# Kernel tuning notes

Measured on AMD Instinct MI355X. Metric: run time of the kernel, lower is better.

Reference implementation:

```python
import jax, jax.numpy as jnp
import numpy as np

T, B, IN, H, L = 512, 64, 1024, 1024, 2


def setup_inputs() -> dict:
    key = jax.random.key(0)
    ks = jax.random.split(key, 9)
    stdv = 1.0 / np.sqrt(H)
    u = lambda k, shape: jax.random.uniform(k, shape, jnp.float32, -stdv, stdv)
    return {
        "x": jax.random.normal(ks[0], (T, B, IN), jnp.float32),
        "h0": jnp.zeros((L, B, H), jnp.float32),
        "w_ih_l0": u(ks[1], (3 * H, IN)),
        "w_hh_l0": u(ks[2], (3 * H, H)),
        "b_ih_l0": u(ks[3], (3 * H,)),
        "b_hh_l0": u(ks[4], (3 * H,)),
        "w_ih_l1": u(ks[5], (3 * H, H)),
        "w_hh_l1": u(ks[6], (3 * H, H)),
        "b_ih_l1": u(ks[7], (3 * H,)),
        "b_hh_l1": u(ks[8], (3 * H,)),
    }


def _gru_layer(x, h, w_ih, w_hh, b_ih, b_hh):
    # Precompute input-side gates for all timesteps: [T, B, 3H]
    gx = jnp.einsum('tbi,gi->tbg', x, w_ih) + b_ih

    def step(h_prev, gx_t):
        gh = h_prev @ w_hh.T + b_hh  # [B, 3H]
        gxr, gxz, gxn = jnp.split(gx_t, 3, axis=-1)
        ghr, ghz, ghn = jnp.split(gh, 3, axis=-1)
        r = jax.nn.sigmoid(gxr + ghr)
        z = jax.nn.sigmoid(gxz + ghz)
        n = jnp.tanh(gxn + r * ghn)
        h_new = n + z * (h_prev - n)
        return h_new, h_new

    h_last, ys = jax.lax.scan(step, h, gx)
    return ys, h_last


def reference(x, h0, w_ih_l0, w_hh_l0, b_ih_l0, b_hh_l0,
              w_ih_l1, w_hh_l1, b_ih_l1, b_hh_l1):
    y0, hn0 = _gru_layer(x, h0[0], w_ih_l0, w_hh_l0, b_ih_l0, b_hh_l0)
    y1, hn1 = _gru_layer(y0, h0[1], w_ih_l1, w_hh_l1, b_ih_l1, b_hh_l1)
    return y1, jnp.stack([hn0, hn1], axis=0)
```

## Files before the change

### kernel.cpp

```cpp
#include <hip/hip_runtime.h>
#include <hip/hip_bf16.h>
#include <math.h>

#define T_STEPS 512
#define BATCH   64
#define HID     1024
#define G3      3072
#define BH      (BATCH * HID)

typedef __attribute__((ext_vector_type(8))) short          bf16x8;
typedef __attribute__((ext_vector_type(8))) unsigned short u16x8;
typedef __attribute__((ext_vector_type(4))) float          f32x4;

__device__ inline unsigned short f2bf(float f) {
    __hip_bfloat16 h = __float2bfloat16(f);
    return *reinterpret_cast<unsigned short*>(&h);
}

__device__ inline bf16x8 load_h8(const unsigned short* p) {
    typedef unsigned long long u64;
    u64 lo = __hip_atomic_load((const u64*)p,       __ATOMIC_RELAXED, __HIP_MEMORY_SCOPE_AGENT);
    u64 hi = __hip_atomic_load((const u64*)(p + 4), __ATOMIC_RELAXED, __HIP_MEMORY_SCOPE_AGENT);
    union { u64 q[2]; bf16x8 v; } u;
    u.q[0] = lo; u.q[1] = hi;
    return u.v;
}

__device__ inline float fast_sigmoid(float x) {
    return __builtin_amdgcn_rcpf(1.f + __expf(-x));
}
__device__ inline float fast_tanh(float x) {
    float e = __expf(-2.f * fabsf(x));
    float t = (1.f - e) * __builtin_amdgcn_rcpf(1.f + e);
    return copysignf(t, x);
}

__global__ void cvt_f32_bf16(const float* __restrict__ src,
                             unsigned short* __restrict__ dst, int n)
{
    int i = (blockIdx.x * blockDim.x + threadIdx.x) * 4;
    if (i + 3 < n) {
        float4 v = *(const float4*)(src + i);
        ushort4 o;
        o.x = f2bf(v.x); o.y = f2bf(v.y); o.z = f2bf(v.z); o.w = f2bf(v.w);
        *(ushort4*)(dst + i) = o;
    }
}

__global__ __launch_bounds__(256) void gemm_gx_bf16(
    const float* __restrict__ A, const unsigned short* __restrict__ Wbf,
    const float* __restrict__ bias, float* __restrict__ C, int M)
{
    __shared__ unsigned short As[128][72];
    __shared__ unsigned short Bs[128][72];
    const int tid = threadIdx.x;
    const int l  = tid & 63;
    const int w  = tid >> 6;
    const int wm = w >> 1, wn = w & 1;
    const int m0 = blockIdx.y * 128, n0 = blockIdx.x * 128;
    const int lr = l & 15, lk = (l >> 4) * 8;

    f32x4 acc[4][4] = {};

    const int arow = tid >> 4, acol = (tid & 15) * 4;
    const int brow = tid >> 3, bcol = (tid & 7) * 8;

    for (int k0 = 0; k0 < 1024; k0 += 64) {
        float4 av[8];
        #pragma unroll
        for (int r = 0; r < 8; ++r)
            av[r] = *(const float4*)(A + (size_t)(m0 + r * 16 + arow) * 1024 + k0 + acol);
        u16x8 bv[4];
        #pragma unroll
        for (int r = 0; r < 4; ++r)
            bv[r] = *(const u16x8*)(Wbf + (size_t)(n0 + r * 32 + brow) * 1024 + k0 + bcol);

        __syncthreads();
        #pragma unroll
        for (int r = 0; r < 8; ++r) {
            ushort4 o;
            o.x = f2bf(av[r].x); o.y = f2bf(av[r].y);
            o.z = f2bf(av[r].z); o.w = f2bf(av[r].w);
            *(ushort4*)&As[r * 16 + arow][acol] = o;
        }
        #pragma unroll
        for (int r = 0; r < 4; ++r)
            *(u16x8*)&Bs[r * 32 + brow][bcol] = bv[r];
        __syncthreads();

        #pragma unroll
        for (int kk = 0; kk < 2; ++kk) {
            bf16x8 af[4], bfr[4];
            #pragma unroll
            for (int i = 0; i < 4; ++i)
                af[i] = *(const bf16x8*)&As[wm * 64 + i * 16 + lr][kk * 32 + lk];
            #pragma unroll
            for (int j = 0; j < 4; ++j)
                bfr[j] = *(const bf16x8*)&Bs[wn * 64 + j * 16 + lr][kk * 32 + lk];
            #pragma unroll
            for (int i = 0; i < 4; ++i)
                #pragma unroll
                for (int j = 0; j < 4; ++j)
                    acc[i][j] = __builtin_amdgcn_mfma_f32_16x16x32_bf16(
                        af[i], bfr[j], acc[i][j], 0, 0, 0);
        }
    }

    #pragma unroll
    for (int j = 0; j < 4; ++j) {
        const int col = n0 + wn * 64 + j * 16 + lr;
        const float bv = bias[col];
        #pragma unroll
        for (int i = 0; i < 4; ++i) {
            const int rb = m0 + wm * 64 + i * 16 + (l >> 4) * 4;
            #pragma unroll
            for (int r = 0; r < 4; ++r)
                C[(size_t)(rb + r) * G3 + col] = acc[i][j][r] + bv;
        }
    }
}

__global__ __launch_bounds__(256, 1) void gru_persist(
    const float* __restrict__ gx,
    unsigned short* __restrict__ hbf,
    const float* __restrict__ hprev0,
    const unsigned short* __restrict__ whh,
    const float* __restrict__ bhh,
    float* __restrict__ y_all,
    unsigned int* __restrict__ flags,
    int step_base, int t0, int tc)
{
    __shared__ float red[4][64][13];

    const int tid = threadIdx.x;
    const int bid = blockIdx.x;
    const int jt = bid & 63;
    const int bg = bid >> 6;
    const int l  = tid & 63;
    const int w  = tid >> 6;
    const int lr = l & 15, lk = (l >> 4) * 8;

    const unsigned short* hpb = hbf + (size_t)(bg * 16 + lr) * HID + w * 256 + lk;
    const unsigned short* wr  = whh + (size_t)(jt * 16 + lr) * HID + w * 256 + lk;
    const unsigned short* wz  = wr + (size_t)HID * HID;
    const unsigned short* wn  = wz + (size_t)HID * HID;

    bf16x8 wvr[8], wvz[8], wvn[8];
    #pragma unroll
    for (int kc = 0; kc < 8; ++kc) {
        wvr[kc] = *(const bf16x8*)(wr + kc * 32);
        wvz[kc] = *(const bf16x8*)(wz + kc * 32);
        wvn[kc] = *(const bf16x8*)(wn + kc * 32);
    }

    const int q  = tid >> 6;
    const int fl = tid & 63;
    const int j  = jt * 16 + (fl & 15);
    const int b  = bg * 16 + 4 * (fl >> 4) + q;
    const float brc = bhh[j], bzc = bhh[HID + j], bnc = bhh[2 * HID + j];
    float hreg = hprev0[(size_t)b * HID + j];

    float gxr = gx[(size_t)b * G3 + j];
    float gxz = gx[(size_t)b * G3 + HID + j];
    float gxn = gx[(size_t)b * G3 + 2 * HID + j];

    for (int ts = 0; ts < tc; ++ts) {
        const int t = t0 + ts;
        const size_t coff = (size_t)(t & 1) * BH;
        const size_t noff = (size_t)((t + 1) & 1) * BH;
        const unsigned int stamp = (unsigned int)(step_base + ts + 1);

        f32x4 ar = {0.f, 0.f, 0.f, 0.f};
        f32x4 az = {0.f, 0.f, 0.f, 0.f};
        f32x4 an = {0.f, 0.f, 0.f, 0.f};
        #pragma unroll
        for (int kc = 0; kc < 8; ++kc) {
            bf16x8 a = load_h8(hpb + coff + kc * 32);
            ar = __builtin_amdgcn_mfma_f32_16x16x32_bf16(a, wvr[kc], ar, 0, 0, 0);
            az = __builtin_amdgcn_mfma_f32_16x16x32_bf16(a, wvz[kc], az, 0, 0, 0);
            an = __builtin_amdgcn_mfma_f32_16x16x32_bf16(a, wvn[kc], an, 0, 0, 0);
        }
        #pragma unroll
        for (int i = 0; i < 4; ++i) {
            red[w][l][i]     = ar[i];
            red[w][l][4 + i] = az[i];
            red[w][l][8 + i] = an[i];
        }
        __syncthreads();

        float sr = 0.f, sz = 0.f, sn = 0.f;
        #pragma unroll
        for (int s = 0; s < 4; ++s) {
            sr += red[s][fl][q];
            sz += red[s][fl][4 + q];
            sn += red[s][fl][8 + q];
        }
        const float rg = fast_sigmoid(gxr + sr + brc);
        const float zg = fast_sigmoid(gxz + sz + bzc);
        const float ng = fast_tanh(gxn + rg * (sn + bnc));
        hreg = ng + zg * (hreg - ng);

        unsigned int myu = (unsigned int)f2bf(hreg);
        unsigned int pu  = __shfl_xor(myu, 1);
        if (!(fl & 1))
            __hip_atomic_store((unsigned int*)(hbf + noff + (size_t)b * HID + j),
                               myu | (pu << 16),
                               __ATOMIC_RELAXED, __HIP_MEMORY_SCOPE_AGENT);

        __syncthreads();
        if (tid == 0)
            __hip_atomic_store(&flags[bg * 64 + jt], stamp,
                               __ATOMIC_RELAXED, __HIP_MEMORY_SCOPE_AGENT);

        y_all[(size_t)t * BH + (size_t)b * HID + j] = hreg;
        const int tsn = (ts + 1 < tc) ? ts + 1 : ts;
        const float* gxp = gx + (size_t)tsn * BATCH * G3;
        const float ngxr = gxp[(size_t)b * G3 + j];
        const float ngxz = gxp[(size_t)b * G3 + HID + j];
        const float ngxn = gxp[(size_t)b * G3 + 2 * HID + j];

        if (tid < 64) {
            for (;;) {
                unsigned int f = __hip_atomic_load(&flags[bg * 64 + tid],
                                                   __ATOMIC_RELAXED,
                                                   __HIP_MEMORY_SCOPE_AGENT);
                if (__ballot(f >= stamp) == ~0ull) break;
                __builtin_amdgcn_s_sleep(1);
            }
        }
        __syncthreads();
        gxr = ngxr; gxz = ngxz; gxn = ngxn;
    }
}

__global__ void copy_f32(const float* __restrict__ src, float* __restrict__ dst, int n)
{
    int i = blockIdx.x * blockDim.x + threadIdx.x;
    if (i < n) dst[i] = src[i];
}

extern "C" void kernel_launch(void* const* d_in, const int* in_sizes, int n_in,
                              void* d_out, int out_size, void* d_ws, size_t ws_size,
                              hipStream_t stream)
{
    const float* x    = (const float*)d_in[0];
    const float* h0   = (const float*)d_in[1];
    const float* wih[2] = {(const float*)d_in[2], (const float*)d_in[6]};
    const float* whh[2] = {(const float*)d_in[3], (const float*)d_in[7]};
    const float* bih[2] = {(const float*)d_in[4], (const float*)d_in[8]};
    const float* bhh[2] = {(const float*)d_in[5], (const float*)d_in[9]};

    float* out = (float*)d_out;
    float* y   = out;
    float* hn  = out + (size_t)T_STEPS * BH;

    const size_t WSZ = (size_t)G3 * HID;
    unsigned short* wsu = (unsigned short*)d_ws;
    unsigned short* whh_bf[2] = {wsu, wsu + WSZ};
    unsigned short* wih_bf[2] = {wsu + 2 * WSZ, wsu + 3 * WSZ};
    unsigned short* hbf = wsu + 4 * WSZ;
    unsigned int* flags = (unsigned int*)(wsu + 4 * WSZ + 2 * (size_t)BH);
    const size_t FLAG_N = 4 * 64;
    float* gx = (float*)((char*)flags + FLAG_N * sizeof(unsigned int));
    const size_t fixed_bytes = (4 * WSZ + 2 * (size_t)BH) * 2 + FLAG_N * 4;
    const size_t gx_bytes = ws_size > fixed_bytes ? ws_size - fixed_bytes : 0;

    int TC = 512;
    while (TC > 2 && (size_t)TC * BATCH * G3 * 4 > gx_bytes) TC >>= 1;

    hipMemsetAsync(flags, 0, FLAG_N * sizeof(unsigned int), stream);

    for (int layer = 0; layer < 2; ++layer) {
        cvt_f32_bf16<<<(int)(WSZ / 1024), 256, 0, stream>>>(whh[layer], whh_bf[layer], (int)WSZ);
        cvt_f32_bf16<<<(int)(WSZ / 1024), 256, 0, stream>>>(wih[layer], wih_bf[layer], (int)WSZ);
    }

    for (int layer = 0; layer < 2; ++layer) {
        const float* A_all = (layer == 0) ? x : y;
        const float* hinit = h0 + (size_t)layer * BH;

        cvt_f32_bf16<<<BH / 1024, 256, 0, stream>>>(hinit, hbf, BH);

        for (int c0 = 0; c0 < T_STEPS; c0 += TC) {
            dim3 ggrid(G3 / 128, TC * BATCH / 128);
            gemm_gx_bf16<<<ggrid, 256, 0, stream>>>(
                A_all + (size_t)c0 * BH, wih_bf[layer], bih[layer],
                gx, TC * BATCH);

            const float* gxp = gx;
            const float* hprev0 = (c0 == 0) ? hinit : (y + (size_t)(c0 - 1) * BH);
            const unsigned short* whhp = whh_bf[layer];
            const float* bhhp = bhh[layer];
            float* yp = y;
            unsigned short* hbfp = hbf;
            unsigned int* flp = flags;
            int sb = layer * T_STEPS + c0;
            int t0v = c0, tcv = TC;
            void* kargs[] = {(void*)&gxp, (void*)&hbfp, (void*)&hprev0,
                             (void*)&whhp, (void*)&bhhp, (void*)&yp,
                             (void*)&flp, (void*)&sb, (void*)&t0v, (void*)&tcv};
            hipLaunchCooperativeKernel((const void*)gru_persist,
                                       dim3(256), dim3(256), kargs, 0, stream);
        }
        copy_f32<<<(BH + 255) / 256, 256, 0, stream>>>(
            y + (size_t)(T_STEPS - 1) * BH, hn + (size_t)layer * BH, BH);
    }
}
```

Baseline: 5.778 ms.

## Stage recurrent weights in LDS and use lighter custom barriers in GRU loop

The recurrent weight tiles for each block, previously held in registers (72 VGPRs per lane), are now staged once into shared memory and read from LDS on every timestep. The __syncthreads calls in the step loop become raw s_barrier calls with explicit waitcnt, so a barrier only waits on the counter it actually needs. This frees registers and cuts barrier overhead, at the cost of extra LDS reads on the critical recurrent path. The weaker fences also rely on the vmcnt wait before the flag store to keep the h writes ordered ahead of the flag.

After: 7.546 ms. 1.31x slower.

```diff
diff --git a/kernel.cpp b/kernel.cpp
--- a/kernel.cpp
+++ b/kernel.cpp
@@ -11,6 +11,7 @@
 typedef __attribute__((ext_vector_type(8))) short          bf16x8;
 typedef __attribute__((ext_vector_type(8))) unsigned short u16x8;
 typedef __attribute__((ext_vector_type(4))) float          f32x4;
+typedef unsigned long long u64;
 
 __device__ inline unsigned short f2bf(float f) {
     __hip_bfloat16 h = __float2bfloat16(f);
@@ -18,7 +19,6 @@
 }
 
 __device__ inline bf16x8 load_h8(const unsigned short* p) {
-    typedef unsigned long long u64;
     u64 lo = __hip_atomic_load((const u64*)p,       __ATOMIC_RELAXED, __HIP_MEMORY_SCOPE_AGENT);
     u64 hi = __hip_atomic_load((const u64*)(p + 4), __ATOMIC_RELAXED, __HIP_MEMORY_SCOPE_AGENT);
     union { u64 q[2]; bf16x8 v; } u;
@@ -33,6 +33,16 @@
     float e = __expf(-2.f * fabsf(x));
     float t = (1.f - e) * __builtin_amdgcn_rcpf(1.f + e);
     return copysignf(t, x);
+}
+
+__device__ inline void bar_lgkm() {
+    asm volatile("s_waitcnt lgkmcnt(0)" ::: "memory");
+    __builtin_amdgcn_s_barrier();
+    __builtin_amdgcn_sched_barrier(0);
+}
+__device__ inline void bar_only() {
+    __builtin_amdgcn_s_barrier();
+    __builtin_amdgcn_sched_barrier(0);
 }
 
 __global__ void cvt_f32_bf16(const float* __restrict__ src,
@@ -130,39 +140,47 @@
     unsigned int* __restrict__ flags,
     int step_base, int t0, int tc)
 {
+    __shared__ unsigned short wlds[3 * 4 * 8 * 4 * 16 * 8];
     __shared__ float red[4][64][13];
 
     const int tid = threadIdx.x;
     const int bid = blockIdx.x;
     const int jt = bid & 63;
     const int bg = bid >> 6;
-    const int l  = tid & 63;
-    const int w  = tid >> 6;
-    const int lr = l & 15, lk = (l >> 4) * 8;
-
-    const unsigned short* hpb = hbf + (size_t)(bg * 16 + lr) * HID + w * 256 + lk;
-    const unsigned short* wr  = whh + (size_t)(jt * 16 + lr) * HID + w * 256 + lk;
-    const unsigned short* wz  = wr + (size_t)HID * HID;
-    const unsigned short* wn  = wz + (size_t)HID * HID;
-
-    bf16x8 wvr[8], wvz[8], wvn[8];
+    const int l   = tid & 63;
+    const int ks  = tid >> 6;
+    const int lr  = l & 15;
+    const int lgrp = l >> 4;
+
     #pragma unroll
-    for (int kc = 0; kc < 8; ++kc) {
-        wvr[kc] = *(const bf16x8*)(wr + kc * 32);
-        wvz[kc] = *(const bf16x8*)(wz + kc * 32);
-        wvn[kc] = *(const bf16x8*)(wn + kc * 32);
-    }
+    for (int i = 0; i < 24; ++i) {
+        int vi  = tid + i * 256;
+        int slr = vi & 15;
+        int slg = (vi >> 4) & 3;
+        int skc = (vi >> 6) & 7;
+        int sks = (vi >> 9) & 3;
+        int sg  = vi >> 11;
+        u16x8 wv = *(const u16x8*)(whh
+            + ((size_t)(sg * HID + jt * 16 + slr) << 10)
+            + sks * 256 + skc * 32 + slg * 8);
+        *(u16x8*)&wlds[(size_t)vi * 8] = wv;
+    }
+
+    const unsigned short* hpb = hbf + (size_t)(bg * 16 + lr) * HID + ks * 256 + lgrp * 8;
+    const int wbase = (ks * 8) * 64 + lgrp * 16 + lr;
 
     const int q  = tid >> 6;
     const int fl = tid & 63;
     const int j  = jt * 16 + (fl & 15);
     const int b  = bg * 16 + 4 * (fl >> 4) + q;
-    const float brc = bhh[j], bzc = bhh[HID + j], bnc = bhh[2 * HID + j];
+    const float bhr = bhh[j], bhz = bhh[HID + j], bhn = bhh[2 * HID + j];
     float hreg = hprev0[(size_t)b * HID + j];
 
     float gxr = gx[(size_t)b * G3 + j];
     float gxz = gx[(size_t)b * G3 + HID + j];
     float gxn = gx[(size_t)b * G3 + 2 * HID + j];
+
+    bar_lgkm();
 
     for (int ts = 0; ts < tc; ++ts) {
         const int t = t0 + ts;
@@ -175,18 +193,21 @@
         f32x4 an = {0.f, 0.f, 0.f, 0.f};
         #pragma unroll
         for (int kc = 0; kc < 8; ++kc) {
-            bf16x8 a = load_h8(hpb + coff + kc * 32);
-            ar = __builtin_amdgcn_mfma_f32_16x16x32_bf16(a, wvr[kc], ar, 0, 0, 0);
-            az = __builtin_amdgcn_mfma_f32_16x16x32_bf16(a, wvz[kc], az, 0, 0, 0);
-            an = __builtin_amdgcn_mfma_f32_16x16x32_bf16(a, wvn[kc], an, 0, 0, 0);
+            bf16x8 a  = load_h8(hpb + coff + kc * 32);
+            bf16x8 Br = *(const bf16x8*)&wlds[(size_t)(wbase + kc * 64) * 8];
+            bf16x8 Bz = *(const bf16x8*)&wlds[(size_t)(2048 + wbase + kc * 64) * 8];
+            bf16x8 Bn = *(const bf16x8*)&wlds[(size_t)(4096 + wbase + kc * 64) * 8];
+            ar = __builtin_amdgcn_mfma_f32_16x16x32_bf16(a, Br, ar, 0, 0, 0);
+            az = __builtin_amdgcn_mfma_f32_16x16x32_bf16(a, Bz, az, 0, 0, 0);
+            an = __builtin_amdgcn_mfma_f32_16x16x32_bf16(a, Bn, an, 0, 0, 0);
         }
         #pragma unroll
         for (int i = 0; i < 4; ++i) {
-            red[w][l][i]     = ar[i];
-            red[w][l][4 + i] = az[i];
-            red[w][l][8 + i] = an[i];
-        }
-        __syncthreads();
+            red[ks][l][i]     = ar[i];
+            red[ks][l][4 + i] = az[i];
+            red[ks][l][8 + i] = an[i];
+        }
+        bar_lgkm();
 
         float sr = 0.f, sz = 0.f, sn = 0.f;
         #pragma unroll
@@ -195,9 +216,9 @@
             sz += red[s][fl][4 + q];
             sn += red[s][fl][8 + q];
         }
-        const float rg = fast_sigmoid(gxr + sr + brc);
-        const float zg = fast_sigmoid(gxz + sz + bzc);
-        const float ng = fast_tanh(gxn + rg * (sn + bnc));
+        const float rg = fast_sigmoid(gxr + sr + bhr);
+        const float zg = fast_sigmoid(gxz + sz + bhz);
+        const float ng = fast_tanh(gxn + rg * (sn + bhn));
         hreg = ng + zg * (hreg - ng);
 
         unsigned int myu = (unsigned int)f2bf(hreg);
@@ -207,7 +228,8 @@
                                myu | (pu << 16),
                                __ATOMIC_RELAXED, __HIP_MEMORY_SCOPE_AGENT);
 
-        __syncthreads();
+        asm volatile("s_waitcnt vmcnt(0)" ::: "memory");
+        bar_only();
         if (tid == 0)
             __hip_atomic_store(&flags[bg * 64 + jt], stamp,
                                __ATOMIC_RELAXED, __HIP_MEMORY_SCOPE_AGENT);
@@ -228,7 +250,7 @@
                 __builtin_amdgcn_s_sleep(1);
             }
         }
-        __syncthreads();
+        bar_only();
         gxr = ngxr; gxz = ngxz; gxn = ngxn;
     }
 }
```

## Fuse both GRU layers into one wavefront-pipelined persistent kernel

Applied to the files above, without the earlier changes.

Replaces the two per-layer persistent recurrences with a single cooperative kernel in which layer 1 runs one timestep behind layer 0. This roughly halves the number of serial grid-wide barrier steps. Layer 1's input projection is computed inline from the bf16 layer-0 hidden state with MFMA, so the second large input GEMM disappears. In exchange, recurrent weights are no longer kept in registers and are reloaded from memory every step, which adds per-step memory traffic and more MFMA work per step. Final hidden states are written directly, and chunk-boundary state is carried through workspace buffers.

New measurement: 7.957 ms. 37.7% more time.

```diff
diff --git a/kernel.cpp b/kernel.cpp
--- a/kernel.cpp
+++ b/kernel.cpp
@@ -11,6 +11,7 @@
 typedef __attribute__((ext_vector_type(8))) short          bf16x8;
 typedef __attribute__((ext_vector_type(8))) unsigned short u16x8;
 typedef __attribute__((ext_vector_type(4))) float          f32x4;
+typedef unsigned long long u64;
 
 __device__ inline unsigned short f2bf(float f) {
     __hip_bfloat16 h = __float2bfloat16(f);
@@ -18,7 +19,6 @@
 }
 
 __device__ inline bf16x8 load_h8(const unsigned short* p) {
-    typedef unsigned long long u64;
     u64 lo = __hip_atomic_load((const u64*)p,       __ATOMIC_RELAXED, __HIP_MEMORY_SCOPE_AGENT);
     u64 hi = __hip_atomic_load((const u64*)(p + 4), __ATOMIC_RELAXED, __HIP_MEMORY_SCOPE_AGENT);
     union { u64 q[2]; bf16x8 v; } u;
@@ -120,101 +120,174 @@
     }
 }
 
-__global__ __launch_bounds__(256, 1) void gru_persist(
-    const float* __restrict__ gx,
-    unsigned short* __restrict__ hbf,
-    const float* __restrict__ hprev0,
-    const unsigned short* __restrict__ whh,
-    const float* __restrict__ bhh,
-    float* __restrict__ y_all,
+__global__ __launch_bounds__(256, 1) void gru_pipe(
+    const float* __restrict__ gx0,
+    unsigned short* __restrict__ hbf0,
+    unsigned short* __restrict__ hbf1,
+    const float* __restrict__ h0f_in,
+    const float* __restrict__ h1f_in,
+    float* __restrict__ h0f_out,
+    float* __restrict__ h1f_out,
+    const unsigned short* __restrict__ whh0,
+    const unsigned short* __restrict__ wih1,
+    const unsigned short* __restrict__ whh1,
+    const float* __restrict__ bhh0,
+    const float* __restrict__ bih1,
+    const float* __restrict__ bhh1,
+    float* __restrict__ y1_all,
+    float* __restrict__ hn,
     unsigned int* __restrict__ flags,
-    int step_base, int t0, int tc)
+    int c0, int tc)
 {
-    __shared__ float red[4][64][13];
+    __shared__ float red[4][64][29];
 
     const int tid = threadIdx.x;
     const int bid = blockIdx.x;
     const int jt = bid & 63;
     const int bg = bid >> 6;
-    const int l  = tid & 63;
-    const int w  = tid >> 6;
-    const int lr = l & 15, lk = (l >> 4) * 8;
-
-    const unsigned short* hpb = hbf + (size_t)(bg * 16 + lr) * HID + w * 256 + lk;
-    const unsigned short* wr  = whh + (size_t)(jt * 16 + lr) * HID + w * 256 + lk;
-    const unsigned short* wz  = wr + (size_t)HID * HID;
-    const unsigned short* wn  = wz + (size_t)HID * HID;
-
-    bf16x8 wvr[8], wvz[8], wvn[8];
-    #pragma unroll
-    for (int kc = 0; kc < 8; ++kc) {
-        wvr[kc] = *(const bf16x8*)(wr + kc * 32);
-        wvz[kc] = *(const bf16x8*)(wz + kc * 32);
-        wvn[kc] = *(const bf16x8*)(wn + kc * 32);
-    }
+    const int l   = tid & 63;
+    const int ks  = tid >> 6;
+    const int lr  = l & 15;
+    const int lgrp = l >> 4;
+
+    const unsigned short* hpb0 = hbf0 + (size_t)(bg * 16 + lr) * HID + ks * 256 + lgrp * 8;
+    const unsigned short* hpb1 = hbf1 + (size_t)(bg * 16 + lr) * HID + ks * 256 + lgrp * 8;
+
+    const size_t basew = ((size_t)(jt * 16 + lr) << 10) + ks * 256 + lgrp * 8;
+    const size_t GS = (size_t)HID * HID;
+    const unsigned short* w0 = whh0 + basew;
+    const unsigned short* wi = wih1 + basew;
+    const unsigned short* wh = whh1 + basew;
 
     const int q  = tid >> 6;
     const int fl = tid & 63;
     const int j  = jt * 16 + (fl & 15);
     const int b  = bg * 16 + 4 * (fl >> 4) + q;
-    const float brc = bhh[j], bzc = bhh[HID + j], bnc = bhh[2 * HID + j];
-    float hreg = hprev0[(size_t)b * HID + j];
-
-    float gxr = gx[(size_t)b * G3 + j];
-    float gxz = gx[(size_t)b * G3 + HID + j];
-    float gxn = gx[(size_t)b * G3 + 2 * HID + j];
-
-    for (int ts = 0; ts < tc; ++ts) {
-        const int t = t0 + ts;
-        const size_t coff = (size_t)(t & 1) * BH;
-        const size_t noff = (size_t)((t + 1) & 1) * BH;
-        const unsigned int stamp = (unsigned int)(step_base + ts + 1);
-
-        f32x4 ar = {0.f, 0.f, 0.f, 0.f};
-        f32x4 az = {0.f, 0.f, 0.f, 0.f};
-        f32x4 an = {0.f, 0.f, 0.f, 0.f};
-        #pragma unroll
-        for (int kc = 0; kc < 8; ++kc) {
-            bf16x8 a = load_h8(hpb + coff + kc * 32);
-            ar = __builtin_amdgcn_mfma_f32_16x16x32_bf16(a, wvr[kc], ar, 0, 0, 0);
-            az = __builtin_amdgcn_mfma_f32_16x16x32_bf16(a, wvz[kc], az, 0, 0, 0);
-            an = __builtin_amdgcn_mfma_f32_16x16x32_bf16(a, wvn[kc], an, 0, 0, 0);
-        }
-        #pragma unroll
-        for (int i = 0; i < 4; ++i) {
-            red[w][l][i]     = ar[i];
-            red[w][l][4 + i] = az[i];
-            red[w][l][8 + i] = an[i];
-        }
-        __syncthreads();
-
-        float sr = 0.f, sz = 0.f, sn = 0.f;
+    const float b0r = bhh0[j], b0z = bhh0[HID + j], b0n = bhh0[2 * HID + j];
+    const float b1r = bih1[j] + bhh1[j];
+    const float b1z = bih1[HID + j] + bhh1[HID + j];
+    const float b1ni = bih1[2 * HID + j];
+    const float b1nh = bhh1[2 * HID + j];
+
+    float hreg0 = h0f_in[(size_t)b * HID + j];
+    float hreg1 = h1f_in[(size_t)b * HID + j];
+
+    float gxr = gx0[(size_t)b * G3 + j];
+    float gxz = gx0[(size_t)b * G3 + HID + j];
+    float gxn = gx0[(size_t)b * G3 + 2 * HID + j];
+
+    for (int ts = 0; ts <= tc; ++ts) {
+        const int t0 = c0 + ts;
+        const int t1 = t0 - 1;
+        const bool L0act = (ts < tc);
+        const bool L1act = (ts > 0);
+        const size_t coff0 = (size_t)(t0 & 1) * BH;
+        const size_t noff0 = (size_t)((t0 + 1) & 1) * BH;
+        const size_t coff1 = (size_t)(t1 & 1) * BH;
+        const size_t noff1 = (size_t)((t1 + 1) & 1) * BH;
+        const unsigned int stamp = (unsigned int)(c0 + ts + 1);
+
+        bf16x8 a0v[8];
+        #pragma unroll
+        for (int kc = 0; kc < 8; ++kc)
+            a0v[kc] = load_h8(hpb0 + coff0 + kc * 32);
+
+        f32x4 ar0 = {0.f,0.f,0.f,0.f}, az0 = {0.f,0.f,0.f,0.f}, an0 = {0.f,0.f,0.f,0.f};
+        f32x4 ar1 = {0.f,0.f,0.f,0.f}, az1 = {0.f,0.f,0.f,0.f};
+        f32x4 ani = {0.f,0.f,0.f,0.f}, anh = {0.f,0.f,0.f,0.f};
+
+        if (L0act) {
+            #pragma unroll
+            for (int kc = 0; kc < 8; ++kc) {
+                ar0 = __builtin_amdgcn_mfma_f32_16x16x32_bf16(a0v[kc], *(const bf16x8*)(w0 + kc * 32),          ar0, 0, 0, 0);
+                az0 = __builtin_amdgcn_mfma_f32_16x16x32_bf16(a0v[kc], *(const bf16x8*)(w0 + GS + kc * 32),     az0, 0, 0, 0);
+                an0 = __builtin_amdgcn_mfma_f32_16x16x32_bf16(a0v[kc], *(const bf16x8*)(w0 + 2 * GS + kc * 32), an0, 0, 0, 0);
+            }
+        }
+        if (L1act) {
+            #pragma unroll
+            for (int kc = 0; kc < 8; ++kc) {
+                bf16x8 a1 = load_h8(hpb1 + coff1 + kc * 32);
+                ar1 = __builtin_amdgcn_mfma_f32_16x16x32_bf16(a0v[kc], *(const bf16x8*)(wi + kc * 32),          ar1, 0, 0, 0);
+                az1 = __builtin_amdgcn_mfma_f32_16x16x32_bf16(a0v[kc], *(const bf16x8*)(wi + GS + kc * 32),     az1, 0, 0, 0);
+                ani = __builtin_amdgcn_mfma_f32_16x16x32_bf16(a0v[kc], *(const bf16x8*)(wi + 2 * GS + kc * 32), ani, 0, 0, 0);
+                ar1 = __builtin_amdgcn_mfma_f32_16x16x32_bf16(a1,      *(const bf16x8*)(wh + kc * 32),          ar1, 0, 0, 0);
+                az1 = __builtin_amdgcn_mfma_f32_16x16x32_bf16(a1,      *(const bf16x8*)(wh + GS + kc * 32),     az1, 0, 0, 0);
+                anh = __builtin_amdgcn_mfma_f32_16x16x32_bf16(a1,      *(const bf16x8*)(wh + 2 * GS + kc * 32), anh, 0, 0, 0);
+            }
+        }
+
+        if (L0act) {
+            #pragma unroll
+            for (int i = 0; i < 4; ++i) {
+                red[ks][l][i]      = ar0[i];
+                red[ks][l][4 + i]  = az0[i];
+                red[ks][l][8 + i]  = an0[i];
+            }
+        }
+        if (L1act) {
+            #pragma unroll
+            for (int i = 0; i < 4; ++i) {
+                red[ks][l][12 + i] = ar1[i];
+                red[ks][l][16 + i] = az1[i];
+                red[ks][l][20 + i] = ani[i];
+                red[ks][l][24 + i] = anh[i];
+            }
+        }
+        __syncthreads();
+
+        float sr0 = 0.f, sz0 = 0.f, sn0 = 0.f;
+        float sr1 = 0.f, sz1 = 0.f, sni = 0.f, snh = 0.f;
         #pragma unroll
         for (int s = 0; s < 4; ++s) {
-            sr += red[s][fl][q];
-            sz += red[s][fl][4 + q];
-            sn += red[s][fl][8 + q];
-        }
-        const float rg = fast_sigmoid(gxr + sr + brc);
-        const float zg = fast_sigmoid(gxz + sz + bzc);
-        const float ng = fast_tanh(gxn + rg * (sn + bnc));
-        hreg = ng + zg * (hreg - ng);
-
-        unsigned int myu = (unsigned int)f2bf(hreg);
-        unsigned int pu  = __shfl_xor(myu, 1);
-        if (!(fl & 1))
-            __hip_atomic_store((unsigned int*)(hbf + noff + (size_t)b * HID + j),
-                               myu | (pu << 16),
-                               __ATOMIC_RELAXED, __HIP_MEMORY_SCOPE_AGENT);
+            sr0 += red[s][fl][q];       sz0 += red[s][fl][4 + q];  sn0 += red[s][fl][8 + q];
+            sr1 += red[s][fl][12 + q];  sz1 += red[s][fl][16 + q];
+            sni += red[s][fl][20 + q];  snh += red[s][fl][24 + q];
+        }
+
+        if (L0act) {
+            const float rg = fast_sigmoid(gxr + sr0 + b0r);
+            const float zg = fast_sigmoid(gxz + sz0 + b0z);
+            const float ng = fast_tanh(gxn + rg * (sn0 + b0n));
+            hreg0 = ng + zg * (hreg0 - ng);
+            unsigned int myu = (unsigned int)f2bf(hreg0);
+            unsigned int pu  = __shfl_xor(myu, 1);
+            if (!(fl & 1))
+                __hip_atomic_store((unsigned int*)(hbf0 + noff0 + (size_t)b * HID + j),
+                                   myu | (pu << 16),
+                                   __ATOMIC_RELAXED, __HIP_MEMORY_SCOPE_AGENT);
+        }
+        if (L1act) {
+            const float rg = fast_sigmoid(sr1 + b1r);
+            const float zg = fast_sigmoid(sz1 + b1z);
+            const float ng = fast_tanh(sni + b1ni + rg * (snh + b1nh));
+            hreg1 = ng + zg * (hreg1 - ng);
+            unsigned int myu = (unsigned int)f2bf(hreg1);
+            unsigned int pu  = __shfl_xor(myu, 1);
+            if (!(fl & 1))
+                __hip_atomic_store((unsigned int*)(hbf1 + noff1 + (size_t)b * HID + j),
+                                   myu | (pu << 16),
+                                   __ATOMIC_RELAXED, __HIP_MEMORY_SCOPE_AGENT);
+        }
 
         __syncthreads();
         if (tid == 0)
             __hip_atomic_store(&flags[bg * 64 + jt], stamp,
                                __ATOMIC_RELAXED, __HIP_MEMORY_SCOPE_AGENT);
 
-        y_all[(size_t)t * BH + (size_t)b * HID + j] = hreg;
-        const int tsn = (ts + 1 < tc) ? ts + 1 : ts;
-        const float* gxp = gx + (size_t)tsn * BATCH * G3;
+        if (L1act)
+            y1_all[(size_t)t1 * BH + (size_t)b * HID + j] = hreg1;
+        if (L0act && t0 == T_STEPS - 1)
+            hn[(size_t)b * HID + j] = hreg0;
+        if (L1act && t1 == T_STEPS - 1)
+            hn[(size_t)BH + (size_t)b * HID + j] = hreg1;
+        if (ts == tc - 1)
+            h0f_out[(size_t)b * HID + j] = hreg0;
+        if (ts == tc)
+            h1f_out[(size_t)b * HID + j] = hreg1;
+
+        const int tsn = (ts + 1 < tc) ? ts + 1 : (tc - 1);
+        const float* gxp = gx0 + (size_t)tsn * BATCH * G3;
         const float ngxr = gxp[(size_t)b * G3 + j];
         const float ngxz = gxp[(size_t)b * G3 + HID + j];
         const float ngxn = gxp[(size_t)b * G3 + 2 * HID + j];
@@ -233,22 +306,20 @@
     }
 }
 
-__global__ void copy_f32(const float* __restrict__ src, float* __restrict__ dst, int n)
-{
-    int i = blockIdx.x * blockDim.x + threadIdx.x;
-    if (i < n) dst[i] = src[i];
-}
-
 extern "C" void kernel_launch(void* const* d_in, const int* in_sizes, int n_in,
                               void* d_out, int out_size, void* d_ws, size_t ws_size,
                               hipStream_t stream)
 {
     const float* x    = (const float*)d_in[0];
     const float* h0   = (const float*)d_in[1];
-    const float* wih[2] = {(const float*)d_in[2], (const float*)d_in[6]};
-    const float* whh[2] = {(const float*)d_in[3], (const float*)d_in[7]};
-    const float* bih[2] = {(const float*)d_in[4], (const float*)d_in[8]};
-    const float* bhh[2] = {(const float*)d_in[5], (const float*)d_in[9]};
+    const float* wih0 = (const float*)d_in[2];
+    const float* whh0 = (const float*)d_in[3];
+    const float* bih0 = (const float*)d_in[4];
+    const float* bhh0 = (const float*)d_in[5];
+    const float* wih1 = (const float*)d_in[6];
+    const float* whh1 = (const float*)d_in[7];
+    const float* bih1 = (const float*)d_in[8];
+    const float* bhh1 = (const float*)d_in[9];
 
     float* out = (float*)d_out;
     float* y   = out;
@@ -256,13 +327,19 @@
 
     const size_t WSZ = (size_t)G3 * HID;
     unsigned short* wsu = (unsigned short*)d_ws;
-    unsigned short* whh_bf[2] = {wsu, wsu + WSZ};
-    unsigned short* wih_bf[2] = {wsu + 2 * WSZ, wsu + 3 * WSZ};
-    unsigned short* hbf = wsu + 4 * WSZ;
-    unsigned int* flags = (unsigned int*)(wsu + 4 * WSZ + 2 * (size_t)BH);
+    unsigned short* whh0_bf = wsu;
+    unsigned short* wih0_bf = wsu + WSZ;
+    unsigned short* wih1_bf = wsu + 2 * WSZ;
+    unsigned short* whh1_bf = wsu + 3 * WSZ;
+    unsigned short* hbf0 = wsu + 4 * WSZ;
+    unsigned short* hbf1 = hbf0 + 2 * (size_t)BH;
+    unsigned int* flags = (unsigned int*)(hbf1 + 2 * (size_t)BH);
     const size_t FLAG_N = 4 * 64;
-    float* gx = (float*)((char*)flags + FLAG_N * sizeof(unsigned int));
-    const size_t fixed_bytes = (4 * WSZ + 2 * (size_t)BH) * 2 + FLAG_N * 4;
+    float* h0carry = (float*)((char*)flags + FLAG_N * sizeof(unsigned int));
+    float* h1carry = h0carry + BH;
+    float* gx = h1carry + BH;
+    const size_t fixed_bytes = 4 * WSZ * 2 + 4 * (size_t)BH * 2
+                             + FLAG_N * 4 + 2 * (size_t)BH * 4;
     const size_t gx_bytes = ws_size > fixed_bytes ? ws_size - fixed_bytes : 0;
 
     int TC = 512;
@@ -270,39 +347,43 @@
 
     hipMemsetAsync(flags, 0, FLAG_N * sizeof(unsigned int), stream);
 
-    for (int layer = 0; layer < 2; ++layer) {
-        cvt_f32_bf16<<<(int)(WSZ / 1024), 256, 0, stream>>>(whh[layer], whh_bf[layer], (int)WSZ);
-        cvt_f32_bf16<<<(int)(WSZ / 1024), 256, 0, stream>>>(wih[layer], wih_bf[layer], (int)WSZ);
-    }
-
-    for (int layer = 0; layer < 2; ++layer) {
-        const float* A_all = (layer == 0) ? x : y;
-        const float* hinit = h0 + (size_t)layer * BH;
-
-        cvt_f32_bf16<<<BH / 1024, 256, 0, stream>>>(hinit, hbf, BH);
-
-        for (int c0 = 0; c0 < T_STEPS; c0 += TC) {
-            dim3 ggrid(G3 / 128, TC * BATCH / 128);
-            gemm_gx_bf16<<<ggrid, 256, 0, stream>>>(
-                A_all + (size_t)c0 * BH, wih_bf[layer], bih[layer],
-                gx, TC * BATCH);
-
-            const float* gxp = gx;
-            const float* hprev0 = (c0 == 0) ? hinit : (y + (size_t)(c0 - 1) * BH);
-            const unsigned short* whhp = whh_bf[layer];
-            const float* bhhp = bhh[layer];
-            float* yp = y;
-            unsigned short* hbfp = hbf;
-            unsigned int* flp = flags;
-            int sb = layer * T_STEPS + c0;
-            int t0v = c0, tcv = TC;
-            void* kargs[] = {(void*)&gxp, (void*)&hbfp, (void*)&hprev0,
-                             (void*)&whhp, (void*)&bhhp, (void*)&yp,
-                             (void*)&flp, (void*)&sb, (void*)&t0v, (void*)&tcv};
-            hipLaunchCooperativeKernel((const void*)gru_persist,
-                                       dim3(256), dim3(256), kargs, 0, stream);
-        }
-        copy_f32<<<(BH + 255) / 256, 256, 0, stream>>>(
-            y + (size_t)(T_STEPS - 1) * BH, hn + (size_t)layer * BH, BH);
-    }
-}
+    cvt_f32_bf16<<<(int)(WSZ / 1024), 256, 0, stream>>>(whh0, whh0_bf, (int)WSZ);
+    cvt_f32_bf16<<<(int)(WSZ / 1024), 256, 0, stream>>>(wih0, wih0_bf, (int)WSZ);
+    cvt_f32_bf16<<<(int)(WSZ / 1024), 256, 0, stream>>>(wih1, wih1_bf, (int)WSZ);
+    cvt_f32_bf16<<<(int)(WSZ / 1024), 256, 0, stream>>>(whh1, whh1_bf, (int)WSZ);
+
+    cvt_f32_bf16<<<BH / 1024, 256, 0, stream>>>(h0, hbf0, BH);
+    cvt_f32_bf16<<<BH / 1024, 256, 0, stream>>>(h0 + BH, hbf1, BH);
+
+    for (int c0 = 0; c0 < T_STEPS; c0 += TC) {
+        dim3 ggrid(G3 / 128, TC * BATCH / 128);
+        gemm_gx_bf16<<<ggrid, 256, 0, stream>>>(
+            x + (size_t)c0 * BH, wih0_bf, bih0, gx, TC * BATCH);
+
+        const float* gxp = gx;
+        const float* h0fi = (c0 == 0) ? h0 : h0carry;
+        const float* h1fi = (c0 == 0) ? (h0 + BH) : h1carry;
+        float* h0fo = h0carry;
+        float* h1fo = h1carry;
+        const unsigned short* w0p = whh0_bf;
+        const unsigned short* wip = wih1_bf;
+        const unsigned short* whp = whh1_bf;
+        const float* b0p = bhh0;
+        const float* bip = bih1;
+        const float* bhp = bhh1;
+        float* yp = y;
+        float* hnp = hn;
+        unsigned short* hb0 = hbf0;
+        unsigned short* hb1 = hbf1;
+        unsigned int* flp = flags;
+        int c0v = c0, tcv = TC;
+        void* kargs[] = {(void*)&gxp, (void*)&hb0, (void*)&hb1,
+                         (void*)&h0fi, (void*)&h1fi, (void*)&h0fo, (void*)&h1fo,
+                         (void*)&w0p, (void*)&wip, (void*)&whp,
+                         (void*)&b0p, (void*)&bip, (void*)&bhp,
+                         (void*)&yp, (void*)&hnp, (void*)&flp,
+                         (void*)&c0v, (void*)&tcv};
+        hipLaunchCooperativeKernel((const void*)gru_pipe,
+                                   dim3(256), dim3(256), kargs, 0, stream);
+    }
+}
```
